# Kernel tuning notes

Measured on AMD Instinct MI355X. Metric: run time of the kernel, lower is better.

## Reference

```python
import jax, jax.numpy as jnp
import numpy as np

L, H, C, V, T_MAX = 12, 12, 768, 50257, 1024
D = C // H
LN_EPS = 1e-5


def layer_norm(x, w, b):
    m = jnp.mean(x, axis=-1, keepdims=True)
    v = jnp.mean(jnp.square(x - m), axis=-1, keepdims=True)
    return (x - m) * jax.lax.rsqrt(v + LN_EPS) * w + b


def setup_inputs() -> dict:
    key = jax.random.key(0)
    ks = jax.random.split(key, 16)
    B, T = 2, 1024
    s = 0.02
    inp = {
        "idx": jax.random.randint(ks[0], (B, T), 0, V),
        "wte": jax.random.normal(ks[1], (V, C), jnp.float32) * s,
        "wpe": jax.random.normal(ks[2], (T_MAX, C), jnp.float32) * s,
        # stacked per-layer params, leading axis = layer
        "ln1_w": jnp.ones((L, C), jnp.float32),
        "ln1_b": jnp.zeros((L, C), jnp.float32),
        "Wq": jax.random.normal(ks[3], (L, C, C), jnp.float32) * s,
        "bq": jnp.zeros((L, C), jnp.float32),
        "Wk": jax.random.normal(ks[4], (L, C, C), jnp.float32) * s,
        "bk": jnp.zeros((L, C), jnp.float32),
        "Wv": jax.random.normal(ks[5], (L, C, C), jnp.float32) * s,
        "bv": jnp.zeros((L, C), jnp.float32),
        "Wo": jax.random.normal(ks[6], (L, C, C), jnp.float32) * (s / np.sqrt(2 * L)),
        "bo": jnp.zeros((L, C), jnp.float32),
        "ln2_w": jnp.ones((L, C), jnp.float32),
        "ln2_b": jnp.zeros((L, C), jnp.float32),
        "Wfc": jax.random.normal(ks[7], (L, C, 4 * C), jnp.float32) * s,
        "bfc": jnp.zeros((L, 4 * C), jnp.float32),
        "Wpr": jax.random.normal(ks[8], (L, 4 * C, C), jnp.float32) * (s / np.sqrt(2 * L)),
        "bpr": jnp.zeros((L, C), jnp.float32),
        "ln_f_w": jnp.ones((C,), jnp.float32),
        "ln_f_b": jnp.zeros((C,), jnp.float32),
        "Wlm": jax.random.normal(ks[9], (C, V), jnp.float32) * s,
    }
    return inp


def _forward(idx, wte, wpe, ln1_w, ln1_b, Wq, bq, Wk, bk, Wv, bv, Wo, bo,
             ln2_w, ln2_b, Wfc, bfc, Wpr, bpr, ln_f_w, ln_f_b, Wlm):
    B, T = idx.shape
    x = wte[idx] + wpe[jnp.arange(T)][None, :, :]  # (B,T,C)
    causal = jnp.tril(jnp.ones((T, T), bool))  # (T,T) causal mask
    scale = 1.0 / np.sqrt(D)
    neg_inf = jnp.finfo(x.dtype).min

    def block(x, p):
        (l1w, l1b, wq, bq_, wk, bk_, wv, bv_, wo, bo_,
         l2w, l2b, wfc, bfc_, wpr, bpr_) = p
        h = layer_norm(x, l1w, l1b)
        q = (h @ wq + bq_).reshape(B, T, H, D)
        k = (h @ wk + bk_).reshape(B, T, H, D)
        v = (h @ wv + bv_).reshape(B, T, H, D)
        scores = jnp.einsum("bqhd,bkhd->bhqk", q, k) * scale
        scores = jnp.where(causal[None, None], scores, neg_inf)
        attn = jax.nn.softmax(scores, axis=-1)
        y = jnp.einsum("bhqk,bkhd->bqhd", attn, v).reshape(B, T, C)
        x = x + y @ wo + bo_
        h2 = layer_norm(x, l2w, l2b)
        x = x + jax.nn.gelu(h2 @ wfc + bfc_, approximate=False) @ wpr + bpr_
        return x, None

    params = (ln1_w, ln1_b, Wq, bq, Wk, bk, Wv, bv, Wo, bo,
              ln2_w, ln2_b, Wfc, bfc, Wpr, bpr)
    x, _ = jax.lax.scan(block, x, params)
    x = layer_norm(x, ln_f_w, ln_f_b)
    logits = x @ Wlm  # (B,T,V)
    return logits


def reference(idx, wte, wpe, ln1_w, ln1_b, Wq, bq, Wk, bk, Wv, bv, Wo, bo,
              ln2_w, ln2_b, Wfc, bfc, Wpr, bpr, ln_f_w, ln_f_b, Wlm):
    return _forward(idx, wte, wpe, ln1_w, ln1_b, Wq, bq, Wk, bk, Wv, bv, Wo, bo,
                    ln2_w, ln2_b, Wfc, bfc, Wpr, bpr, ln_f_w, ln_f_b, Wlm)
```

## Files before the change

### kernel.cpp

```cpp
#include <hip/hip_runtime.h>
#include <math.h>
#include <cstddef>


#define Cdim 768
#define Hn   12
#define Ln   12
#define Tn   1024
#define Bn   2
#define Mrows (Bn * Tn)

typedef unsigned short ushort_t;
typedef __bf16 bf16x8 __attribute__((ext_vector_type(8)));
typedef float  f32x4  __attribute__((ext_vector_type(4)));

__device__ __forceinline__ ushort_t f2bf(float v) {
    union { float f; unsigned int u; } x; x.f = v;
    unsigned int r = x.u + 0x7fffu + ((x.u >> 16) & 1u);
    return (ushort_t)(r >> 16);
}
__device__ __forceinline__ float gelu_f(float v) {
    return 0.5f * v * (1.0f + erff(v * 0.70710678118654752f));
}
__device__ __forceinline__ void gload16(const void* g, void* l) {
    __builtin_amdgcn_global_load_lds(
        (const __attribute__((address_space(1))) unsigned int*)g,
        (__attribute__((address_space(3))) unsigned int*)l, 16, 0, 0);
}

__global__ void embed_k(const int* __restrict__ idx, const float* __restrict__ wte,
                        const float* __restrict__ wpe, float* __restrict__ x) {
    int i = blockIdx.x * 256 + threadIdx.x;
    int c  = i % Cdim;
    int bt = i / Cdim;
    int t  = bt % Tn;
    int tok = idx[bt];
    x[i] = wte[(size_t)tok * Cdim + c] + wpe[(size_t)t * Cdim + c];
}

__global__ __launch_bounds__(256) void ln_k(const float* __restrict__ x,
                                            const float* __restrict__ w,
                                            const float* __restrict__ b,
                                            ushort_t* __restrict__ out) {
    int row = blockIdx.x;
    const float* xr = x + (size_t)row * Cdim;
    int t = threadIdx.x;
    float v0 = xr[t], v1 = xr[t + 256], v2 = xr[t + 512];
    float s = v0 + v1 + v2;
    #pragma unroll
    for (int o = 32; o > 0; o >>= 1) s += __shfl_xor(s, o);
    __shared__ float red[8];
    int wid = t >> 6;
    if ((t & 63) == 0) red[wid] = s;
    __syncthreads();
    float mean = (red[0] + red[1] + red[2] + red[3]) * (1.0f / 768.0f);
    float d0 = v0 - mean, d1 = v1 - mean, d2 = v2 - mean;
    float sq = d0 * d0 + d1 * d1 + d2 * d2;
    #pragma unroll
    for (int o = 32; o > 0; o >>= 1) sq += __shfl_xor(sq, o);
    if ((t & 63) == 0) red[4 + wid] = sq;
    __syncthreads();
    float var = (red[4] + red[5] + red[6] + red[7]) * (1.0f / 768.0f);
    float rstd = rsqrtf(var + 1e-5f);
    ushort_t* orow = out + (size_t)row * Cdim;
    orow[t]       = f2bf(d0 * rstd * w[t]       + b[t]);
    orow[t + 256] = f2bf(d1 * rstd * w[t + 256] + b[t + 256]);
    orow[t + 512] = f2bf(d2 * rstd * w[t + 512] + b[t + 512]);
}

__device__ __forceinline__ void tconv_tile(const float* __restrict__ W,
                                           ushort_t* __restrict__ WT,
                                           int K, int N, int n0, int k0, bool guard) {
    __shared__ float t[32][33];
    int x = threadIdx.x & 31, y = threadIdx.x >> 5;
    #pragma unroll
    for (int j = 0; j < 4; ++j) {
        int kk = k0 + y + j * 8, nn = n0 + x;
        t[y + j * 8][x] = (!guard || nn < N) ? W[(size_t)kk * N + nn] : 0.0f;
    }
    __syncthreads();
    #pragma unroll
    for (int j = 0; j < 4; ++j) {
        int nn = n0 + y + j * 8, kk = k0 + x;
        WT[(size_t)nn * K + kk] = f2bf(t[x][y + j * 8]);
    }
}

__global__ __launch_bounds__(256) void wconv_k(const float* __restrict__ W,
                                               ushort_t* __restrict__ WT,
                                               int K, int N) {
    tconv_tile(W, WT, K, N, blockIdx.x * 32, blockIdx.y * 32, true);
}

__global__ __launch_bounds__(256) void conv_layer_k(
    const float* __restrict__ Wq, const float* __restrict__ Wk,
    const float* __restrict__ Wv, const float* __restrict__ Wo,
    const float* __restrict__ Wfc, const float* __restrict__ Wpr,
    const float* __restrict__ bq, const float* __restrict__ bk,
    const float* __restrict__ bv,
    ushort_t* __restrict__ wqkvt, ushort_t* __restrict__ wot,
    ushort_t* __restrict__ wfct,  ushort_t* __restrict__ wprt,
    float* __restrict__ bqkv) {
    int bid = blockIdx.x;
    if (bid < 2304) {
        int z = bid / 576, t = bid % 576;
        const float* W = (z == 0) ? Wq : (z == 1) ? Wk : (z == 2) ? Wv : Wo;
        ushort_t* dst = (z < 3) ? (wqkvt + (size_t)z * 768 * 768) : wot;
        tconv_tile(W, dst, 768, 768, (t % 24) * 32, (t / 24) * 32, false);
    } else if (bid < 4608) {
        int t = bid - 2304;
        tconv_tile(Wfc, wfct, 768, 3072, (t % 96) * 32, (t / 96) * 32, false);
    } else if (bid < 6912) {
        int t = bid - 4608;
        tconv_tile(Wpr, wprt, 3072, 768, (t % 24) * 32, (t / 24) * 32, false);
    } else {
        int i = (bid - 6912) * 256 + threadIdx.x;
        bqkv[i] = (i < 768) ? bq[i] : (i < 1536 ? bk[i - 768] : bv[i - 1536]);
    }
}

template <int BM, int BN, int TH, int WGN,
          bool BIAS, bool GELU_, bool RES, bool OUTBF16, bool XCD>
__global__ __launch_bounds__(TH, 2) void gemm_pipe_k(
    const ushort_t* __restrict__ A,
    const ushort_t* __restrict__ Bt,
    const float* __restrict__ bias,
    const float* __restrict__ res,
    void* __restrict__ Cout,
    int M, int N, int K, int cpx, int mtiles) {
    constexpr int SA = BM * 128;
    constexpr int SB = BN * 128;
    constexpr int WM = BM / 2;
    constexpr int WN = BN / WGN;
    constexpr int FM = WM / 16;
    constexpr int FN = WN / 16;
    constexpr int RJ = TH / 8;
    constexpr int JA = BM / RJ;
    constexpr int JB = BN / RJ;
    constexpr int NL = JA + JB;
    static_assert(NL == 4 || NL == 8, "vmcnt immediate");
    __shared__ char lds[2 * (SA + SB)];
    char* Abase = lds;
    char* Bbase = lds + 2 * SA;

    const int tid = threadIdx.x;
    const int lane = tid & 63;
    const int w = tid >> 6;
    const int wr = w / WGN, wc = w % WGN;
    int m0, n0;
    if (XCD) {
        int lid = ((int)blockIdx.x & 7) * cpx + ((int)blockIdx.x >> 3);
        m0 = (lid % mtiles) * BM;
        n0 = (lid / mtiles) * BN;
    } else {
        m0 = blockIdx.y * BM;
        n0 = blockIdx.x * BN;
    }

    f32x4 acc[FM][FN] = {};

    const int srowl = tid >> 3;
    const int sslot = (tid & 7) ^ (srowl & 7);
    const ushort_t* Asrc = A  + (size_t)(m0 + srowl) * K + sslot * 8;
    const ushort_t* Bsrc = Bt + (size_t)(n0 + srowl) * K + sslot * 8;

    auto stageall = [&](int d, int kt) {
        const ushort_t* As = Asrc + kt * 64;
        const ushort_t* Bs = Bsrc + kt * 64;
        #pragma unroll
        for (int j = 0; j < JA; ++j)
            gload16(As + (size_t)(j * RJ) * K, Abase + d * SA + tid * 16 + j * (TH * 16));
        #pragma unroll
        for (int j = 0; j < JB; ++j)
            gload16(Bs + (size_t)(j * RJ) * K, Bbase + d * SB + tid * 16 + j * (TH * 16));
    };
    auto readA = [&](int d, int m, int ks) -> bf16x8 {
        int rl = wr * WM + m * 16 + (lane & 15);
        int s  = ks * 4 + (lane >> 4);
        return *(const bf16x8*)(Abase + d * SA + rl * 128 + ((s ^ (rl & 7)) << 4));
    };
    auto readB = [&](int d, int n, int ks) -> bf16x8 {
        int rl = wc * WN + n * 16 + (lane & 15);
        int s  = ks * 4 + (lane >> 4);
        return *(const bf16x8*)(Bbase + d * SB + rl * 128 + ((s ^ (rl & 7)) << 4));
    };

    const int nt = K >> 6;
    stageall(0, 0);
    for (int kt = 0; kt < nt; ++kt) {
        const int d = kt & 1;
        if (kt + 1 < nt) {
            stageall(d ^ 1, kt + 1);
            if constexpr (NL == 8) asm volatile("s_waitcnt vmcnt(8)" ::: "memory");
            else                   asm volatile("s_waitcnt vmcnt(4)" ::: "memory");
        } else {
            asm volatile("s_waitcnt vmcnt(0)" ::: "memory");
        }
        __builtin_amdgcn_s_barrier();
        asm volatile("" ::: "memory");

        bf16x8 bfr[FN][2];
        #pragma unroll
        for (int n = 0; n < FN; ++n) {
            bfr[n][0] = readB(d, n, 0);
            bfr[n][1] = readB(d, n, 1);
        }
        __builtin_amdgcn_s_setprio(1);
        #pragma unroll
        for (int m = 0; m < FM; ++m) {
            bf16x8 a0 = readA(d, m, 0);
            bf16x8 a1 = readA(d, m, 1);
            #pragma unroll
            for (int n = 0; n < FN; ++n) {
                acc[m][n] = __builtin_amdgcn_mfma_f32_16x16x32_bf16(
                    a0, bfr[n][0], acc[m][n], 0, 0, 0);
                acc[m][n] = __builtin_amdgcn_mfma_f32_16x16x32_bf16(
                    a1, bfr[n][1], acc[m][n], 0, 0, 0);
            }
        }
        __builtin_amdgcn_s_setprio(0);
        asm volatile("" ::: "memory");
        __builtin_amdgcn_s_barrier();
    }

    const int r0 = (lane >> 4) * 4, c0 = lane & 15;
    #pragma unroll
    for (int m = 0; m < FM; ++m)
        #pragma unroll
        for (int n = 0; n < FN; ++n) {
            int col = n0 + wc * WN + n * 16 + c0;
            if (col < N) {
                #pragma unroll
                for (int q = 0; q < 4; ++q) {
                    int row = m0 + wr * WM + m * 16 + r0 + q;
                    float v = acc[m][n][q];
                    if (BIAS) v += bias[col];
                    if (GELU_) v = gelu_f(v);
                    if (RES) v += res[(size_t)row * N + col];
                    if (OUTBF16) ((ushort_t*)Cout)[(size_t)row * N + col] = f2bf(v);
                    else         ((float*)Cout)[(size_t)row * N + col] = v;
                }
            }
        }
}

__global__ __launch_bounds__(256) void kvprep_k(const ushort_t* __restrict__ qkvb,
                                                ushort_t* __restrict__ kpb,
                                                ushort_t* __restrict__ vtb) {
    __shared__ ushort_t Ls[256][72];
    const int tc = blockIdx.x, h = blockIdx.y, b = blockIdx.z;
    const int tid = threadIdx.x;
    const int tok = tc * 256 + tid;
    const ushort_t* base = qkvb + (size_t)(b * Tn + tok) * 2304 + h * 64;
    ushort_t* kdst = kpb + ((size_t)(b * Hn + h) * Tn + tok) * 64;
    #pragma unroll
    for (int i = 0; i < 8; ++i)
        *(uint4*)&kdst[i * 8] = *(const uint4*)(base + 768 + i * 8);
    #pragma unroll
    for (int i = 0; i < 8; ++i)
        *(uint4*)&Ls[tid][i * 8] = *(const uint4*)(base + 1536 + i * 8);
    __syncthreads();
    const int d = tid & 63, tg = tid >> 6;
    ushort_t tmp[64];
    #pragma unroll
    for (int i = 0; i < 64; ++i) tmp[i] = Ls[tg * 64 + i][d];
    ushort_t* dst = vtb + ((size_t)(b * Hn + h) * 64 + d) * Tn + tc * 256 + tg * 64;
    #pragma unroll
    for (int i = 0; i < 8; ++i)
        *(uint4*)&dst[i * 8] = *(const uint4*)&tmp[i * 8];
}

__global__ __launch_bounds__(256) void attn_mfma_k(
    const ushort_t* __restrict__ qkvb,
    const ushort_t* __restrict__ kpb,
    const ushort_t* __restrict__ vtb,
    ushort_t* __restrict__ yb) {
    __shared__ ushort_t Ks[64][72];
    __shared__ ushort_t Vt[64][72];
    __shared__ ushort_t Pl[4][16][72];
    const int chunk = (Tn / 64 - 1) - blockIdx.x;
    const int h = blockIdx.y, b = blockIdx.z;
    const int tid = threadIdx.x, lane = tid & 63, w = tid >> 6;
    const int c = lane & 15, g = lane >> 4;
    const int qrow0 = chunk * 64 + w * 16;

    const ushort_t* qp = qkvb + (size_t)(b * Tn + qrow0 + c) * 2304 + h * 64 + g * 8;
    bf16x8 qa0 = *(const bf16x8*)qp;
    bf16x8 qa1 = *(const bf16x8*)(qp + 32);

    f32x4 accO[4] = {};
    float mrun[4], lrun[4];
    #pragma unroll
    for (int q = 0; q < 4; ++q) { mrun[q] = -1e30f; lrun[q] = 0.0f; }

    const int skey = tid >> 2, sd0 = (tid & 3) * 16;
    const ushort_t* ksrc = kpb + ((size_t)(b * Hn + h) * Tn + skey) * 64 + sd0;
    const int vd = tid >> 2, vseg = tid & 3;
    const ushort_t* vsrc = vtb + ((size_t)(b * Hn + h) * 64 + vd) * Tn + vseg * 16;
    ushort_t* KsW = &Ks[skey][sd0];
    ushort_t* VtW = &Vt[vd][vseg * 16];

    const int ntiles = chunk + 1;
    for (int kt = 0; kt < ntiles; ++kt) {
        __syncthreads();
        {
            const ushort_t* kp = ksrc + (size_t)kt * 64 * 64;
            *(uint4*)KsW       = *(const uint4*)kp;
            *(uint4*)(KsW + 8) = *(const uint4*)(kp + 8);
            const ushort_t* vp = vsrc + kt * 64;
            *(uint4*)VtW       = *(const uint4*)vp;
            *(uint4*)(VtW + 8) = *(const uint4*)(vp + 8);
        }
        __syncthreads();

        f32x4 sf[4];
        #pragma unroll
        for (int nk = 0; nk < 4; ++nk) {
            bf16x8 kf0 = *(const bf16x8*)&Ks[nk * 16 + c][g * 8];
            bf16x8 kf1 = *(const bf16x8*)&Ks[nk * 16 + c][g * 8 + 32];
            f32x4 z = {};
            z = __builtin_amdgcn_mfma_f32_16x16x32_bf16(qa0, kf0, z, 0, 0, 0);
            z = __builtin_amdgcn_mfma_f32_16x16x32_bf16(qa1, kf1, z, 0, 0, 0);
            sf[nk] = z;
        }
        float pmax[4] = {-1e30f, -1e30f, -1e30f, -1e30f};
        #pragma unroll
        for (int nk = 0; nk < 4; ++nk) {
            int key = kt * 64 + nk * 16 + c;
            #pragma unroll
            for (int q = 0; q < 4; ++q) {
                float sv = sf[nk][q];
                int row = qrow0 + g * 4 + q;
                sv = (key > row) ? -1e30f : sv;
                sf[nk][q] = sv;
                pmax[q] = fmaxf(pmax[q], sv);
            }
        }
        #pragma unroll
        for (int q = 0; q < 4; ++q)
            #pragma unroll
            for (int off = 1; off < 16; off <<= 1)
                pmax[q] = fmaxf(pmax[q], __shfl_xor(pmax[q], off));
        float corr[4], psum[4];
        #pragma unroll
        for (int q = 0; q < 4; ++q) {
            float mn = fmaxf(mrun[q], pmax[q]);
            corr[q] = __expf((mrun[q] - mn) * 0.125f);
            mrun[q] = mn;
            psum[q] = 0.0f;
        }
        #pragma unroll
        for (int nk = 0; nk < 4; ++nk)
            #pragma unroll
            for (int q = 0; q < 4; ++q) {
                float p = __expf((sf[nk][q] - mrun[q]) * 0.125f);
                psum[q] += p;
                Pl[w][g * 4 + q][nk * 16 + c] = f2bf(p);
            }
        #pragma unroll
        for (int q = 0; q < 4; ++q) {
            #pragma unroll
            for (int off = 1; off < 16; off <<= 1)
                psum[q] += __shfl_xor(psum[q], off);
            lrun[q] = lrun[q] * corr[q] + psum[q];
        }
        #pragma unroll
        for (int ni = 0; ni < 4; ++ni)
            #pragma unroll
            for (int q = 0; q < 4; ++q)
                accO[ni][q] *= corr[q];

        asm volatile("" ::: "memory");
        bf16x8 pa0 = *(const bf16x8*)&Pl[w][c][g * 8];
        bf16x8 pa1 = *(const bf16x8*)&Pl[w][c][g * 8 + 32];
        #pragma unroll
        for (int ni = 0; ni < 4; ++ni) {
            bf16x8 bv0 = *(const bf16x8*)&Vt[ni * 16 + c][g * 8];
            bf16x8 bv1 = *(const bf16x8*)&Vt[ni * 16 + c][g * 8 + 32];
            accO[ni] = __builtin_amdgcn_mfma_f32_16x16x32_bf16(pa0, bv0, accO[ni], 0, 0, 0);
            accO[ni] = __builtin_amdgcn_mfma_f32_16x16x32_bf16(pa1, bv1, accO[ni], 0, 0, 0);
        }
    }

    #pragma unroll
    for (int q = 0; q < 4; ++q) {
        float inv = 1.0f / lrun[q];
        ushort_t* yr = yb + (size_t)(b * Tn + qrow0 + g * 4 + q) * Cdim + h * 64;
        #pragma unroll
        for (int ni = 0; ni < 4; ++ni)
            yr[ni * 16 + c] = f2bf(accO[ni][q] * inv);
    }
}

extern "C" void kernel_launch(void* const* d_in, const int* in_sizes, int n_in,
                              void* d_out, int out_size, void* d_ws, size_t ws_size,
                              hipStream_t stream) {
    const int*   idx  = (const int*)d_in[0];
    const float* wte  = (const float*)d_in[1];
    const float* wpe  = (const float*)d_in[2];
    const float* ln1w = (const float*)d_in[3];
    const float* ln1b = (const float*)d_in[4];
    const float* Wq   = (const float*)d_in[5];
    const float* bq   = (const float*)d_in[6];
    const float* Wk   = (const float*)d_in[7];
    const float* bk   = (const float*)d_in[8];
    const float* Wv   = (const float*)d_in[9];
    const float* bv   = (const float*)d_in[10];
    const float* Wo   = (const float*)d_in[11];
    const float* bo   = (const float*)d_in[12];
    const float* ln2w = (const float*)d_in[13];
    const float* ln2b = (const float*)d_in[14];
    const float* Wfc  = (const float*)d_in[15];
    const float* bfc  = (const float*)d_in[16];
    const float* Wpr  = (const float*)d_in[17];
    const float* bpr  = (const float*)d_in[18];
    const float* lnfw = (const float*)d_in[19];
    const float* lnfb = (const float*)d_in[20];
    const float* Wlm  = (const float*)d_in[21];
    float* out = (float*)d_out;

    const int M = Mrows;
    const int V = out_size / M;
    const int Vpad = ((V + 255) / 256) * 256;

    float*    x     = (float*)d_ws;
    float*    bqkv  = x + (size_t)M * Cdim;
    ushort_t* qkvb  = (ushort_t*)(bqkv + 2304);
    ushort_t* kpb   = qkvb + (size_t)M * 2304;
    ushort_t* vtb   = kpb + (size_t)Bn * Hn * Tn * 64;
    ushort_t* hb    = vtb + (size_t)Bn * Hn * 64 * Tn;
    ushort_t* yb    = hb + (size_t)M * Cdim;
    ushort_t* mid   = yb + (size_t)M * Cdim;
    ushort_t* wqkvt = mid + (size_t)M * 3072;
    ushort_t* wot   = wqkvt + (size_t)2304 * Cdim;
    ushort_t* wfct  = wot + (size_t)Cdim * Cdim;
    ushort_t* wprt  = wfct + (size_t)3072 * Cdim;
    ushort_t* wlmt  = wprt + (size_t)Cdim * 3072;

    embed_k<<<(M * Cdim) / 256, 256, 0, stream>>>(idx, wte, wpe, x);

    for (int l = 0; l < Ln; ++l) {
        const size_t wo2 = (size_t)l * Cdim * Cdim;
        const size_t wo4 = (size_t)l * Cdim * 4 * Cdim;
        conv_layer_k<<<6921, 256, 0, stream>>>(
            Wq + wo2, Wk + wo2, Wv + wo2, Wo + wo2, Wfc + wo4, Wpr + wo4,
            bq + l * Cdim, bk + l * Cdim, bv + l * Cdim,
            wqkvt, wot, wfct, wprt, bqkv);

        ln_k<<<M, 256, 0, stream>>>(x, ln1w + l * Cdim, ln1b + l * Cdim, hb);
        gemm_pipe_k<128, 128, 256, 2, true, false, false, true, false>
            <<<dim3(18, 16), 256, 0, stream>>>(
            hb, wqkvt, bqkv, nullptr, qkvb, M, 2304, Cdim, 0, 0);
        kvprep_k<<<dim3(4, Hn, Bn), 256, 0, stream>>>(qkvb, kpb, vtb);
        attn_mfma_k<<<dim3(16, Hn, Bn), 256, 0, stream>>>(qkvb, kpb, vtb, yb);
        gemm_pipe_k<64, 64, 256, 2, true, false, true, false, false>
            <<<dim3(12, 32), 256, 0, stream>>>(
            yb, wot, bo + l * Cdim, x, x, M, Cdim, Cdim, 0, 0);
        ln_k<<<M, 256, 0, stream>>>(x, ln2w + l * Cdim, ln2b + l * Cdim, hb);
        gemm_pipe_k<128, 128, 256, 2, true, true, false, true, false>
            <<<dim3(24, 16), 256, 0, stream>>>(
            hb, wfct, bfc + (size_t)l * 4 * Cdim, nullptr, mid, M, 3072, Cdim, 0, 0);
        gemm_pipe_k<64, 64, 256, 2, true, false, true, false, false>
            <<<dim3(12, 32), 256, 0, stream>>>(
            mid, wprt, bpr + l * Cdim, x, x, M, Cdim, 3072, 0, 0);
    }

    ln_k<<<M, 256, 0, stream>>>(x, lnfw, lnfb, hb);
    wconv_k<<<dim3(Vpad / 32, 24), 256, 0, stream>>>(Wlm, wlmt, Cdim, V);
    const int nblk = 16 * (Vpad / 128);
    gemm_pipe_k<128, 128, 256, 2, false, false, false, false, true>
        <<<nblk, 256, 0, stream>>>(
        hb, wlmt, nullptr, nullptr, out, M, V, Cdim, nblk / 8, 16);
}
```

Baseline: 1.971 ms.

## Fuse K/V layout transform into QKV GEMM epilogue and batch weight conversion

The QKV GEMM epilogue now writes Q row-major, K in per-head token-major layout and V transposed. This removes the separate kvprep kernel and its extra read/write of the QKV buffer. When the workspace is large enough, all layers' weights are converted to bf16 in one launch up front instead of one conversion kernel per layer, which reduces launches and per-layer serialization. The trade-off is that the epilogue K writes become scattered 2-byte stores, and the batched path needs much more workspace.

```diff
diff --git a/kernel.cpp b/kernel.cpp
--- a/kernel.cpp
+++ b/kernel.cpp
@@ -92,16 +92,13 @@
     tconv_tile(W, WT, K, N, blockIdx.x * 32, blockIdx.y * 32, true);
 }
 
-__global__ __launch_bounds__(256) void conv_layer_k(
-    const float* __restrict__ Wq, const float* __restrict__ Wk,
-    const float* __restrict__ Wv, const float* __restrict__ Wo,
-    const float* __restrict__ Wfc, const float* __restrict__ Wpr,
-    const float* __restrict__ bq, const float* __restrict__ bk,
-    const float* __restrict__ bv,
-    ushort_t* __restrict__ wqkvt, ushort_t* __restrict__ wot,
-    ushort_t* __restrict__ wfct,  ushort_t* __restrict__ wprt,
-    float* __restrict__ bqkv) {
-    int bid = blockIdx.x;
+__device__ __forceinline__ void conv_body(
+    int bid,
+    const float* Wq, const float* Wk, const float* Wv, const float* Wo,
+    const float* Wfc, const float* Wpr,
+    const float* bq, const float* bk, const float* bv,
+    ushort_t* wqkvt, ushort_t* wot, ushort_t* wfct, ushort_t* wprt,
+    float* bqkv) {
     if (bid < 2304) {
         int z = bid / 576, t = bid % 576;
         const float* W = (z == 0) ? Wq : (z == 1) ? Wk : (z == 2) ? Wv : Wo;
@@ -119,14 +116,42 @@
     }
 }
 
+__global__ __launch_bounds__(256) void conv_layer_k(
+    const float* Wq, const float* Wk, const float* Wv, const float* Wo,
+    const float* Wfc, const float* Wpr,
+    const float* bq, const float* bk, const float* bv,
+    ushort_t* wqkvt, ushort_t* wot, ushort_t* wfct, ushort_t* wprt,
+    float* bqkv) {
+    conv_body(blockIdx.x, Wq, Wk, Wv, Wo, Wfc, Wpr, bq, bk, bv,
+              wqkvt, wot, wfct, wprt, bqkv);
+}
+
+__global__ __launch_bounds__(256) void conv_all_k(
+    const float* Wq, const float* Wk, const float* Wv, const float* Wo,
+    const float* Wfc, const float* Wpr,
+    const float* bq, const float* bk, const float* bv,
+    ushort_t* wqkvt, ushort_t* wot, ushort_t* wfct, ushort_t* wprt,
+    float* bqkv) {
+    int l = blockIdx.x / 6921, bid = blockIdx.x % 6921;
+    const size_t o2 = (size_t)l * 768 * 768;
+    const size_t o4 = (size_t)l * 768 * 3072;
+    conv_body(bid,
+              Wq + o2, Wk + o2, Wv + o2, Wo + o2, Wfc + o4, Wpr + o4,
+              bq + l * 768, bk + l * 768, bv + l * 768,
+              wqkvt + (size_t)l * 2304 * 768, wot + o2,
+              wfct + o4, wprt + o4, bqkv + l * 2304);
+}
+
 template <int BM, int BN, int TH, int WGN,
-          bool BIAS, bool GELU_, bool RES, bool OUTBF16, bool XCD>
+          bool BIAS, bool GELU_, bool RES, bool OUTBF16, bool XCD, bool QKV>
 __global__ __launch_bounds__(TH, 2) void gemm_pipe_k(
     const ushort_t* __restrict__ A,
     const ushort_t* __restrict__ Bt,
     const float* __restrict__ bias,
     const float* __restrict__ res,
     void* __restrict__ Cout,
+    ushort_t* __restrict__ kdst,
+    ushort_t* __restrict__ vdst,
     int M, int N, int K, int cpx, int mtiles) {
     constexpr int SA = BM * 128;
     constexpr int SB = BN * 128;
@@ -224,6 +249,40 @@
     }
 
     const int r0 = (lane >> 4) * 4, c0 = lane & 15;
+    if constexpr (QKV) {
+        const int region = n0 / 768;
+        #pragma unroll
+        for (int m = 0; m < FM; ++m)
+            #pragma unroll
+            for (int n = 0; n < FN; ++n) {
+                int col = n0 + wc * WN + n * 16 + c0;
+                int row0 = m0 + wr * WM + m * 16 + r0;
+                float vv[4];
+                #pragma unroll
+                for (int q = 0; q < 4; ++q) vv[q] = acc[m][n][q] + bias[col];
+                if (region == 0) {
+                    #pragma unroll
+                    for (int q = 0; q < 4; ++q)
+                        ((ushort_t*)Cout)[(size_t)(row0 + q) * 768 + col] = f2bf(vv[q]);
+                } else if (region == 1) {
+                    int ck = col - 768, h = ck >> 6, dd = ck & 63;
+                    #pragma unroll
+                    for (int q = 0; q < 4; ++q) {
+                        int row = row0 + q;
+                        kdst[(((size_t)(row >> 10) * Hn + h) * Tn + (row & 1023)) * 64 + dd]
+                            = f2bf(vv[q]);
+                    }
+                } else {
+                    int cv = col - 1536, h = cv >> 6, dd = cv & 63;
+                    int bb = row0 >> 10, tok = row0 & 1023;
+                    ushort4 pk;
+                    pk.x = f2bf(vv[0]); pk.y = f2bf(vv[1]);
+                    pk.z = f2bf(vv[2]); pk.w = f2bf(vv[3]);
+                    *(ushort4*)&vdst[(((size_t)bb * Hn + h) * 64 + dd) * Tn + tok] = pk;
+                }
+            }
+        return;
+    }
     #pragma unroll
     for (int m = 0; m < FM; ++m)
         #pragma unroll
@@ -244,34 +303,8 @@
         }
 }
 
-__global__ __launch_bounds__(256) void kvprep_k(const ushort_t* __restrict__ qkvb,
-                                                ushort_t* __restrict__ kpb,
-                                                ushort_t* __restrict__ vtb) {
-    __shared__ ushort_t Ls[256][72];
-    const int tc = blockIdx.x, h = blockIdx.y, b = blockIdx.z;
-    const int tid = threadIdx.x;
-    const int tok = tc * 256 + tid;
-    const ushort_t* base = qkvb + (size_t)(b * Tn + tok) * 2304 + h * 64;
-    ushort_t* kdst = kpb + ((size_t)(b * Hn + h) * Tn + tok) * 64;
-    #pragma unroll
-    for (int i = 0; i < 8; ++i)
-        *(uint4*)&kdst[i * 8] = *(const uint4*)(base + 768 + i * 8);
-    #pragma unroll
-    for (int i = 0; i < 8; ++i)
-        *(uint4*)&Ls[tid][i * 8] = *(const uint4*)(base + 1536 + i * 8);
-    __syncthreads();
-    const int d = tid & 63, tg = tid >> 6;
-    ushort_t tmp[64];
-    #pragma unroll
-    for (int i = 0; i < 64; ++i) tmp[i] = Ls[tg * 64 + i][d];
-    ushort_t* dst = vtb + ((size_t)(b * Hn + h) * 64 + d) * Tn + tc * 256 + tg * 64;
-    #pragma unroll
-    for (int i = 0; i < 8; ++i)
-        *(uint4*)&dst[i * 8] = *(const uint4*)&tmp[i * 8];
-}
-
 __global__ __launch_bounds__(256) void attn_mfma_k(
-    const ushort_t* __restrict__ qkvb,
+    const ushort_t* __restrict__ qb,
     const ushort_t* __restrict__ kpb,
     const ushort_t* __restrict__ vtb,
     ushort_t* __restrict__ yb) {
@@ -284,7 +317,7 @@
     const int c = lane & 15, g = lane >> 4;
     const int qrow0 = chunk * 64 + w * 16;
 
-    const ushort_t* qp = qkvb + (size_t)(b * Tn + qrow0 + c) * 2304 + h * 64 + g * 8;
+    const ushort_t* qp = qb + (size_t)(b * Tn + qrow0 + c) * Cdim + h * 64 + g * 8;
     bf16x8 qa0 = *(const bf16x8*)qp;
     bf16x8 qa1 = *(const bf16x8*)(qp + 32);
 
@@ -423,52 +456,96 @@
     const int V = out_size / M;
     const int Vpad = ((V + 255) / 256) * 256;
 
+    const size_t SZ_QKV = (size_t)2304 * 768;
+    const size_t SZ_O   = (size_t)768 * 768;
+    const size_t SZ_FC  = (size_t)3072 * 768;
+    const size_t SZ_PR  = (size_t)768 * 3072;
+    const size_t SZ_L   = SZ_QKV + SZ_O + SZ_FC + SZ_PR;
+
     float*    x     = (float*)d_ws;
-    float*    bqkv  = x + (size_t)M * Cdim;
-    ushort_t* qkvb  = (ushort_t*)(bqkv + 2304);
-    ushort_t* kpb   = qkvb + (size_t)M * 2304;
+    float*    bqkvb = x + (size_t)M * Cdim;
+    ushort_t* qb    = (ushort_t*)(bqkvb + 12 * 2304);
+    ushort_t* kpb   = qb + (size_t)M * Cdim;
     ushort_t* vtb   = kpb + (size_t)Bn * Hn * Tn * 64;
     ushort_t* hb    = vtb + (size_t)Bn * Hn * 64 * Tn;
     ushort_t* yb    = hb + (size_t)M * Cdim;
     ushort_t* mid   = yb + (size_t)M * Cdim;
-    ushort_t* wqkvt = mid + (size_t)M * 3072;
-    ushort_t* wot   = wqkvt + (size_t)2304 * Cdim;
-    ushort_t* wfct  = wot + (size_t)Cdim * Cdim;
-    ushort_t* wprt  = wfct + (size_t)3072 * Cdim;
-    ushort_t* wlmt  = wprt + (size_t)Cdim * 3072;
+    ushort_t* wlmt  = mid + (size_t)M * 3072;
+    ushort_t* wbase = wlmt + (size_t)Vpad * Cdim;
+
+    const size_t used_common = (size_t)((char*)wbase - (char*)d_ws);
+    const bool big = ws_size >= used_common + 12 * SZ_L * sizeof(ushort_t);
 
     embed_k<<<(M * Cdim) / 256, 256, 0, stream>>>(idx, wte, wpe, x);
-
-    for (int l = 0; l < Ln; ++l) {
-        const size_t wo2 = (size_t)l * Cdim * Cdim;
-        const size_t wo4 = (size_t)l * Cdim * 4 * Cdim;
-        conv_layer_k<<<6921, 256, 0, stream>>>(
-            Wq + wo2, Wk + wo2, Wv + wo2, Wo + wo2, Wfc + wo4, Wpr + wo4,
-            bq + l * Cdim, bk + l * Cdim, bv + l * Cdim,
-            wqkvt, wot, wfct, wprt, bqkv);
-
-        ln_k<<<M, 256, 0, stream>>>(x, ln1w + l * Cdim, ln1b + l * Cdim, hb);
-        gemm_pipe_k<128, 128, 256, 2, true, false, false, true, false>
-            <<<dim3(18, 16), 256, 0, stream>>>(
-            hb, wqkvt, bqkv, nullptr, qkvb, M, 2304, Cdim, 0, 0);
-        kvprep_k<<<dim3(4, Hn, Bn), 256, 0, stream>>>(qkvb, kpb, vtb);
-        attn_mfma_k<<<dim3(16, Hn, Bn), 256, 0, stream>>>(qkvb, kpb, vtb, yb);
-        gemm_pipe_k<64, 64, 256, 2, true, false, true, false, false>
-            <<<dim3(12, 32), 256, 0, stream>>>(
-            yb, wot, bo + l * Cdim, x, x, M, Cdim, Cdim, 0, 0);
-        ln_k<<<M, 256, 0, stream>>>(x, ln2w + l * Cdim, ln2b + l * Cdim, hb);
-        gemm_pipe_k<128, 128, 256, 2, true, true, false, true, false>
-            <<<dim3(24, 16), 256, 0, stream>>>(
-            hb, wfct, bfc + (size_t)l * 4 * Cdim, nullptr, mid, M, 3072, Cdim, 0, 0);
-        gemm_pipe_k<64, 64, 256, 2, true, false, true, false, false>
-            <<<dim3(12, 32), 256, 0, stream>>>(
-            mid, wprt, bpr + l * Cdim, x, x, M, Cdim, 3072, 0, 0);
+    wconv_k<<<dim3(Vpad / 32, 24), 256, 0, stream>>>(Wlm, wlmt, Cdim, V);
+
+    ushort_t* wqkvt0 = wbase;
+    ushort_t* wot0   = wqkvt0 + SZ_QKV;
+    ushort_t* wfct0  = wot0 + SZ_O;
+    ushort_t* wprt0  = wfct0 + SZ_FC;
+    const size_t LSTRIDE = SZ_L;
+
+    if (big) {
+        ushort_t* qkvt_all = wbase;
+        ushort_t* ot_all   = qkvt_all + 12 * SZ_QKV;
+        ushort_t* fct_all  = ot_all + 12 * SZ_O;
+        ushort_t* prt_all  = fct_all + 12 * SZ_FC;
+        conv_all_k<<<12 * 6921, 256, 0, stream>>>(
+            Wq, Wk, Wv, Wo, Wfc, Wpr, bq, bk, bv,
+            qkvt_all, ot_all, fct_all, prt_all, bqkvb);
+        for (int l = 0; l < Ln; ++l) {
+            ushort_t* wqkvt = qkvt_all + (size_t)l * SZ_QKV;
+            ushort_t* wot   = ot_all   + (size_t)l * SZ_O;
+            ushort_t* wfct  = fct_all  + (size_t)l * SZ_FC;
+            ushort_t* wprt  = prt_all  + (size_t)l * SZ_PR;
+            float*    bqkv  = bqkvb + l * 2304;
+            ln_k<<<M, 256, 0, stream>>>(x, ln1w + l * Cdim, ln1b + l * Cdim, hb);
+            gemm_pipe_k<128, 128, 256, 2, true, false, false, true, false, true>
+                <<<dim3(18, 16), 256, 0, stream>>>(
+                hb, wqkvt, bqkv, nullptr, qb, kpb, vtb, M, 2304, Cdim, 0, 0);
+            attn_mfma_k<<<dim3(16, Hn, Bn), 256, 0, stream>>>(qb, kpb, vtb, yb);
+            gemm_pipe_k<64, 64, 256, 2, true, false, true, false, false, false>
+                <<<dim3(12, 32), 256, 0, stream>>>(
+                yb, wot, bo + l * Cdim, x, x, nullptr, nullptr, M, Cdim, Cdim, 0, 0);
+            ln_k<<<M, 256, 0, stream>>>(x, ln2w + l * Cdim, ln2b + l * Cdim, hb);
+            gemm_pipe_k<128, 128, 256, 2, true, true, false, true, false, false>
+                <<<dim3(24, 16), 256, 0, stream>>>(
+                hb, wfct, bfc + (size_t)l * 4 * Cdim, nullptr, mid,
+                nullptr, nullptr, M, 3072, Cdim, 0, 0);
+            gemm_pipe_k<64, 64, 256, 2, true, false, true, false, false, false>
+                <<<dim3(12, 32), 256, 0, stream>>>(
+                mid, wprt, bpr + l * Cdim, x, x, nullptr, nullptr, M, Cdim, 3072, 0, 0);
+        }
+    } else {
+        for (int l = 0; l < Ln; ++l) {
+            const size_t wo2 = (size_t)l * Cdim * Cdim;
+            const size_t wo4 = (size_t)l * Cdim * 4 * Cdim;
+            conv_layer_k<<<6921, 256, 0, stream>>>(
+                Wq + wo2, Wk + wo2, Wv + wo2, Wo + wo2, Wfc + wo4, Wpr + wo4,
+                bq + l * Cdim, bk + l * Cdim, bv + l * Cdim,
+                wqkvt0, wot0, wfct0, wprt0, bqkvb);
+            ln_k<<<M, 256, 0, stream>>>(x, ln1w + l * Cdim, ln1b + l * Cdim, hb);
+            gemm_pipe_k<128, 128, 256, 2, true, false, false, true, false, true>
+                <<<dim3(18, 16), 256, 0, stream>>>(
+                hb, wqkvt0, bqkvb, nullptr, qb, kpb, vtb, M, 2304, Cdim, 0, 0);
+            attn_mfma_k<<<dim3(16, Hn, Bn), 256, 0, stream>>>(qb, kpb, vtb, yb);
+            gemm_pipe_k<64, 64, 256, 2, true, false, true, false, false, false>
+                <<<dim3(12, 32), 256, 0, stream>>>(
+                yb, wot0, bo + l * Cdim, x, x, nullptr, nullptr, M, Cdim, Cdim, 0, 0);
+            ln_k<<<M, 256, 0, stream>>>(x, ln2w + l * Cdim, ln2b + l * Cdim, hb);
+            gemm_pipe_k<128, 128, 256, 2, true, true, false, true, false, false>
+                <<<dim3(24, 16), 256, 0, stream>>>(
+                hb, wfct0, bfc + (size_t)l * 4 * Cdim, nullptr, mid,
+                nullptr, nullptr, M, 3072, Cdim, 0, 0);
+            gemm_pipe_k<64, 64, 256, 2, true, false, true, false, false, false>
+                <<<dim3(12, 32), 256, 0, stream>>>(
+                mid, wprt0, bpr + l * Cdim, x, x, nullptr, nullptr, M, Cdim, 3072, 0, 0);
+        }
     }
 
     ln_k<<<M, 256, 0, stream>>>(x, lnfw, lnfb, hb);
-    wconv_k<<<dim3(Vpad / 32, 24), 256, 0, stream>>>(Wlm, wlmt, Cdim, V);
     const int nblk = 16 * (Vpad / 128);
-    gemm_pipe_k<128, 128, 256, 2, false, false, false, false, true>
+    gemm_pipe_k<128, 128, 256, 2, false, false, false, false, true, false>
         <<<nblk, 256, 0, stream>>>(
-        hb, wlmt, nullptr, nullptr, out, M, V, Cdim, nblk / 8, 16);
-}
+        hb, wlmt, nullptr, nullptr, out, nullptr, nullptr, M, V, Cdim, nblk / 8, 16);
+}
```

Measured after the change: 1.865 ms. 1.06x faster.
